# Performance work log

Hardware: AMD Instinct MI355X
Metric: run time of the kernel (lower is better)

Reference implementation:

```python
import jax, jax.numpy as jnp
import numpy as np

N, M, FEAT, GROUP, EMB = 512, 2048, 1024, 16, 64
DG = FEAT // GROUP  # 64 dims per head


def _make_boxes(k, n):
    k1, k2, k3, k4 = jax.random.split(k, 4)
    x = jax.random.uniform(k1, (n, 1)) * 800.0
    y = jax.random.uniform(k2, (n, 1)) * 800.0
    w = jax.random.uniform(k3, (n, 1)) * 120.0 + 16.0
    h = jax.random.uniform(k4, (n, 1)) * 120.0 + 16.0
    return jnp.concatenate([x, y, x + w, y + h], axis=1)


def setup_inputs() -> dict:
    key = jax.random.key(0)
    ks = jax.random.split(key, 10)
    std = 0.01
    fan = 1.0 / np.sqrt(FEAT).astype(np.float32)
    return {
        "bbox": _make_boxes(ks[0], N),
        "ref_bbox": _make_boxes(ks[1], M),
        "roi_feat": jax.random.normal(ks[2], (N, FEAT), dtype=jnp.float32),
        "ref_feat": jax.random.normal(ks[3], (M, FEAT), dtype=jnp.float32),
        "Wg_w": jax.random.normal(ks[4], (GROUP, EMB)) * std,
        "Wg_b": jnp.zeros((GROUP,), jnp.float32),
        "Wq_w": jax.random.normal(ks[5], (FEAT, FEAT)) * fan,
        "Wq_b": jnp.zeros((FEAT,), jnp.float32),
        "Wk_w": jax.random.normal(ks[6], (FEAT, FEAT)) * fan,
        "Wk_b": jnp.zeros((FEAT,), jnp.float32),
        "Wv_w": jax.random.normal(ks[7], (GROUP, DG, FEAT)) * std,
        "Wv_b": jnp.zeros((FEAT,), jnp.float32),
        "u": jax.random.normal(ks[8], (GROUP, 1, EMB)) * std,
    }


def _position_embedding(bbox, ref_bbox, feat_dim=64, wave_length=1000.0):
    # extract_position_matrix: geometry deltas between every (roi, ref) pair
    xr0, yr0, xr1, yr1 = jnp.split(ref_bbox, 4, axis=1)  # [M,1]
    wr = xr1 - xr0 + 1.0
    hr = yr1 - yr0 + 1.0
    cxr = 0.5 * (xr0 + xr1)
    cyr = 0.5 * (yr0 + yr1)
    x0, y0, x1, y1 = jnp.split(bbox, 4, axis=1)  # [N,1]
    w = x1 - x0 + 1.0
    h = y1 - y0 + 1.0
    cx = 0.5 * (x0 + x1)
    cy = 0.5 * (y0 + y1)
    dx = jnp.log(jnp.abs((cx - cxr.T) / w) + 1e-3)  # [N,M]
    dy = jnp.log(jnp.abs((cy - cyr.T) / h) + 1e-3)
    dw = jnp.log(w / wr.T)
    dh = jnp.log(h / hr.T)
    pos = jnp.stack([dx, dy, dw, dh], axis=2)  # [N,M,4]
    # extract_position_embedding: sinusoidal encoding, feat_dim/8 frequencies
    fr = jnp.arange(feat_dim // 8, dtype=pos.dtype)
    dim_mat = wave_length ** (8.0 / feat_dim * fr)  # [8]
    div = (pos[..., None] * 100.0) / dim_mat  # [N,M,4,8]
    emb = jnp.concatenate([jnp.sin(div), jnp.cos(div)], axis=3)  # [N,M,4,16]
    emb = emb.reshape(emb.shape[0], emb.shape[1], -1)  # [N,M,64]
    return jnp.transpose(emb, (2, 0, 1))  # [emb_dim, N, M]


def reference(bbox, ref_bbox, roi_feat, ref_feat, Wg_w, Wg_b, Wq_w, Wq_b,
              Wk_w, Wk_b, Wv_w, Wv_b, u):
    pe = _position_embedding(bbox, ref_bbox)  # [EMB, N, M]
    # Wg: 1x1 conv over embedding channels, relu -> attention prior weights
    pos_feat = jax.nn.relu(jnp.einsum('ge,enm->gnm', Wg_w, pe)
                           + Wg_b[:, None, None])  # [G,N,M]
    aff_weight = jnp.transpose(pos_feat, (1, 0, 2))  # [N,G,M]
    q = (roi_feat @ Wq_w.T + Wq_b).reshape(-1, GROUP, DG).transpose(1, 0, 2)  # [G,N,DG]
    k = (ref_feat @ Wk_w.T + Wk_b).reshape(-1, GROUP, DG).transpose(1, 0, 2)  # [G,M,DG]
    # content score + global content-bias (u) score, per head
    aff = jnp.einsum('gnd,gmd->gnm', q, k) + jnp.einsum('gld,gmd->glm', u, k)
    aff_scale = (aff / np.sqrt(float(DG))).transpose(1, 0, 2)  # [N,G,M]
    weighted_aff = jnp.log(aff_weight + 1e-6) + aff_scale
    attn = jax.nn.softmax(weighted_aff, axis=2)  # [N,G,M]
    out_t = jnp.einsum('ngm,mf->ngf', attn, ref_feat)  # [N,G,FEAT]
    # grouped 1x1 conv Wv: per-group weight [DG, FEAT]
    out = jnp.einsum('ngc,gdc->ngd', out_t, Wv_w).reshape(-1, FEAT) + Wv_b
    return out  # [N, FEAT]
```

## Files before the change

### kernel.cpp

```cpp
#include <hip/hip_runtime.h>
#include <stdint.h>

typedef float f32x4 __attribute__((ext_vector_type(4)));
typedef _Float16 f16x8 __attribute__((ext_vector_type(8)));
typedef _Float16 f16x4 __attribute__((ext_vector_type(4)));
typedef int int4v __attribute__((ext_vector_type(4)));

#define LOG2E 1.44269504088896340736f

__device__ __forceinline__ void gload_lds16(const void* g, void* l) {
    auto gp = reinterpret_cast<const uint32_t __attribute__((address_space(1)))*>(
        reinterpret_cast<uintptr_t>(g));
    auto lp = reinterpret_cast<uint32_t __attribute__((address_space(3)))*>(
        reinterpret_cast<uintptr_t>(l));
    __builtin_amdgcn_global_load_lds(gp, lp, 16, 0, 0);
}

__global__ __launch_bounds__(256) void mega_prep(
    const float* __restrict__ bbox, const float* __restrict__ ref_bbox,
    const float* __restrict__ roi_feat, const float* __restrict__ ref_feat,
    const float* __restrict__ Wg_w, const float* __restrict__ Wq_w,
    const float* __restrict__ Wk_w, const float* __restrict__ Wv_w,
    const float* __restrict__ Wq_b, const float* __restrict__ uvec,
    _Float16* __restrict__ roi_h, _Float16* __restrict__ ref_h,
    _Float16* __restrict__ wq_h, _Float16* __restrict__ wk_h,
    _Float16* __restrict__ wv_h, _Float16* __restrict__ wg_h,
    float* __restrict__ qbias, float* __restrict__ roig, float* __restrict__ refg)
{
    int idx = blockIdx.x * 256 + threadIdx.x;
    if (idx < 1442048) {
        const float* src; _Float16* dst; int off;
        if (idx < 131072)       { src = roi_feat; dst = roi_h; off = idx; }
        else if (idx < 655360)  { src = ref_feat; dst = ref_h; off = idx - 131072; }
        else if (idx < 917504)  { src = Wq_w;     dst = wq_h;  off = idx - 655360; }
        else if (idx < 1179648) { src = Wk_w;     dst = wk_h;  off = idx - 917504; }
        else if (idx < 1441792) { src = Wv_w;     dst = wv_h;  off = idx - 1179648; }
        else                    { src = Wg_w;     dst = wg_h;  off = idx - 1441792; }
        f32x4 v = *(const f32x4*)(src + (size_t)off * 4);
        f16x4 o;
        o[0] = (_Float16)v[0]; o[1] = (_Float16)v[1];
        o[2] = (_Float16)v[2]; o[3] = (_Float16)v[3];
        *(f16x4*)(dst + (size_t)off * 4) = o;
    } else if (idx < 1442304) {
        int off = idx - 1442048;
        f32x4 a = *(const f32x4*)(Wq_b + off * 4);
        f32x4 b = *(const f32x4*)(uvec + off * 4);
        f32x4 r = a + b;
        *(f32x4*)(qbias + off * 4) = r;
    } else if (idx < 1442816) {
        int n = idx - 1442304;
        f32x4 bb = *(const f32x4*)(bbox + n * 4);
        float w = bb[2] - bb[0] + 1.0f, h = bb[3] - bb[1] + 1.0f;
        f32x4 o1 = {0.5f*(bb[0]+bb[2]), 0.5f*(bb[1]+bb[3]), 1.0f/w, 1.0f/h};
        f32x4 o2 = {__logf(w), __logf(h), 0.f, 0.f};
        *(f32x4*)(roig + n*8) = o1;
        *(f32x4*)(roig + n*8 + 4) = o2;
    } else if (idx < 1444864) {
        int m = idx - 1442816;
        f32x4 bb = *(const f32x4*)(ref_bbox + m * 4);
        float w = bb[2] - bb[0] + 1.0f, h = bb[3] - bb[1] + 1.0f;
        f32x4 o = {0.5f*(bb[0]+bb[2]), 0.5f*(bb[1]+bb[3]), __logf(w), __logf(h)};
        *(f32x4*)(refg + m*4) = o;
    }
}

__global__ __launch_bounds__(256) void mega_gemm(
    const _Float16* __restrict__ roi_h, const _Float16* __restrict__ ref_h,
    const _Float16* __restrict__ wq_h, const _Float16* __restrict__ wk_h,
    const _Float16* __restrict__ wv_h, const float* __restrict__ qbias,
    const float* __restrict__ Wk_b,
    _Float16* __restrict__ Qg, _Float16* __restrict__ Kg, _Float16* __restrict__ Vth)
{
    __shared__ _Float16 As[64 * 32];
    __shared__ _Float16 Bs[128 * 32];

    int b = blockIdx.x;
    const _Float16 *A, *B;
    const float* bias;
    _Float16* out;
    int tm, tn, mode, MR; float scale;
    if (b < 64)       { A = roi_h; B = wq_h; bias = qbias; out = Qg;  tm = b >> 3;        tn = b & 7;       mode = 0; MR = 512;  scale = 0.125f * LOG2E; }
    else if (b < 320) { A = ref_h; B = wk_h; bias = Wk_b;  out = Kg;  tm = (b-64) >> 3;   tn = (b-64) & 7;  mode = 0; MR = 2048; scale = 1.f; }
    else              { A = ref_h; B = wv_h; bias = nullptr; out = Vth; tm = (b-320) >> 3; tn = (b-320) & 7; mode = 1; MR = 2048; scale = 1.f; }

    int tid = threadIdx.x;
    int w = tid >> 6, l = tid & 63, q = l >> 4, t = l & 15;
    int wm = w >> 1, wn = w & 1;
    int m0 = tm * 64, n0 = tn * 128;

    const _Float16* gA  = A + (size_t)(m0 + w*16 + (l >> 2)) * 1024 + (l & 3) * 8;
    const _Float16* gB  = B + (size_t)(n0 + w*16 + (l >> 2)) * 1024 + (l & 3) * 8;
    const _Float16* gB2 = gB + 64 * 1024;
    _Float16* lA  = &As[w * 512];
    _Float16* lB  = &Bs[w * 512];
    _Float16* lB2 = &Bs[2048 + w * 512];

    f32x4 acc[2][4];
    #pragma unroll
    for (int i = 0; i < 2; ++i)
        #pragma unroll
        for (int j = 0; j < 4; ++j)
            acc[i][j] = (f32x4){0.f, 0.f, 0.f, 0.f};

    for (int k0 = 0; k0 < 1024; k0 += 32) {
        gload_lds16(gA + k0, lA);
        gload_lds16(gB + k0, lB);
        gload_lds16(gB2 + k0, lB2);
        __syncthreads();
        f16x8 af[2], bfv[4];
        #pragma unroll
        for (int i = 0; i < 2; ++i)
            af[i]  = *(const f16x8*)&As[(wm*32 + i*16 + t) * 32 + q*8];
        #pragma unroll
        for (int j = 0; j < 4; ++j)
            bfv[j] = *(const f16x8*)&Bs[(wn*64 + j*16 + t) * 32 + q*8];
        #pragma unroll
        for (int mi = 0; mi < 2; ++mi)
            #pragma unroll
            for (int ni = 0; ni < 4; ++ni)
                acc[mi][ni] = __builtin_amdgcn_mfma_f32_16x16x32_f16(af[mi], bfv[ni], acc[mi][ni], 0, 0, 0);
        __syncthreads();
    }

    #pragma unroll
    for (int mi = 0; mi < 2; ++mi) {
        #pragma unroll
        for (int ni = 0; ni < 4; ++ni) {
            int col  = n0 + wn*64 + ni*16 + t;
            int row0 = m0 + wm*32 + mi*16 + q*4;
            f32x4 a = acc[mi][ni];
            if (mode == 0) {
                float bb = bias[col];
                _Float16* op = out + ((size_t)(col >> 6) * MR + row0) * 64 + (col & 63);
                #pragma unroll
                for (int r = 0; r < 4; ++r)
                    op[(size_t)r * 64] = (_Float16)((a[r] + bb) * scale);
            } else {
                f16x4 pk;
                pk[0] = (_Float16)a[0]; pk[1] = (_Float16)a[1];
                pk[2] = (_Float16)a[2]; pk[3] = (_Float16)a[3];
                *(f16x4*)(out + (size_t)col * 2048 + row0) = pk;
            }
        }
    }
}

__global__ __launch_bounds__(256) void mega_prior(
    const _Float16* __restrict__ wg_h, const float* __restrict__ Wg_b,
    const float* __restrict__ roig, const float* __restrict__ refg,
    _Float16* __restrict__ prior)
{
    int tid = threadIdx.x;
    int w = tid >> 6, l = tid & 63, q = l >> 4, p = l & 15;
    int n = blockIdx.x >> 1, half = blockIdx.x & 1;

    f16x8 wa0 = *(const f16x8*)(wg_h + p*64 + q*8);
    f16x8 wa1 = *(const f16x8*)(wg_h + p*64 + 32 + q*8);
    f32x4 wb = *(const f32x4*)(Wg_b + q*4);

    f32x4 rg1 = *(const f32x4*)(roig + n*8);
    f32x4 rg2 = *(const f32x4*)(roig + n*8 + 4);

    float cf[8];
    #pragma unroll
    for (int f = 0; f < 8; ++f)
        cf[f] = 15.9154943091895336f * __builtin_exp2f(-1.24572303558276059f * (float)f);

    float coff = (q & 1) ? 0.25f : 0.0f;
    bool isX = (q < 2);

    int mstart = half * 1024 + w * 256;
    for (int it = 0; it < 16; ++it) {
        int m = mstart + it * 16 + p;
        f32x4 rg = *(const f32x4*)(refg + m * 4);
        float posA = isX ? __logf(fabsf(rg1[0] - rg[0]) * rg1[2] + 1e-3f)
                         : __logf(fabsf(rg1[1] - rg[1]) * rg1[3] + 1e-3f);
        float posB = isX ? (rg2[0] - rg[2]) : (rg2[1] - rg[3]);
        f16x8 e0, e1;
        #pragma unroll
        for (int f = 0; f < 8; ++f) {
            float a0 = posA * cf[f] + coff; a0 -= floorf(a0);
            float a1 = posB * cf[f] + coff; a1 -= floorf(a1);
            e0[f] = (_Float16)__builtin_amdgcn_sinf(a0);
            e1[f] = (_Float16)__builtin_amdgcn_sinf(a1);
        }
        f32x4 acc = wb;
        acc = __builtin_amdgcn_mfma_f32_16x16x32_f16(wa0, e0, acc, 0, 0, 0);
        acc = __builtin_amdgcn_mfma_f32_16x16x32_f16(wa1, e1, acc, 0, 0, 0);
        _Float16* pp = prior + (size_t)n * 2048 + m;
        #pragma unroll
        for (int r = 0; r < 4; ++r)
            pp[(size_t)(q*4 + r) * 1048576] = (_Float16)fmaxf(acc[r], 0.f);
    }
}

#define SWZ(row, cb) ((cb) ^ (((row) & 7) << 4))

__device__ __forceinline__ f16x8 ld128s(const _Float16* base, int row, int cb) {
    return *(const f16x8*)((const char*)base + row * 128 + SWZ(row, cb));
}
__device__ __forceinline__ f16x4 ld64s(const _Float16* base, int row, int cb) {
    return *(const f16x4*)((const char*)base + row * 128 + SWZ(row, cb));
}

__global__ __launch_bounds__(256, 4) void mega_attn(
    const _Float16* __restrict__ Qg, const _Float16* __restrict__ Kg,
    const _Float16* __restrict__ Vth, const _Float16* __restrict__ prior,
    float* __restrict__ Opart, float* __restrict__ Mpart, float* __restrict__ Lpart)
{
    __shared__ __align__(16) _Float16 Kl[4096];
    __shared__ __align__(16) _Float16 Vl[4096];
    __shared__ __align__(16) _Float16 Pl[4096];

    int bid = blockIdx.x;
    int g = bid >> 6, nt4 = (bid >> 3) & 7, s = bid & 7;
    int tid = threadIdx.x;
    int w = tid >> 6, l = tid & 63, q = l >> 4, t = l & 15;
    int n0 = nt4 * 64, m0 = s * 256;

    int n = n0 + w * 16 + t;
    const _Float16* Qrow = Qg + ((size_t)g * 512 + n) * 64;
    f16x8 qf0 = *(const f16x8*)(Qrow + q * 8);
    f16x8 qf1 = *(const f16x8*)(Qrow + 32 + q * 8);

    int r_lo = tid >> 3, c8 = tid & 7;
    const char* gK = (const char*)(Kg + ((size_t)g * 2048 + m0) * 64);
    const char* gV = (const char*)(Vth + (size_t)g * 64 * 2048 + m0);
    const char* gP = (const char*)(prior + ((size_t)g * 512 + n0) * 2048 + m0);

    int4v kr0, kr1, vr0, vr1, pq0, pq1;
#define LOADC(c) { \
    kr0 = *(const int4v*)(gK + (c)*8192 + r_lo*128 + c8*16); \
    kr1 = *(const int4v*)(gK + (c)*8192 + (r_lo+32)*128 + c8*16); \
    vr0 = *(const int4v*)(gV + (c)*128 + (size_t)r_lo*4096 + c8*16); \
    vr1 = *(const int4v*)(gV + (c)*128 + (size_t)(r_lo+32)*4096 + c8*16); \
    pq0 = *(const int4v*)(gP + (c)*128 + (size_t)r_lo*4096 + c8*16); \
    pq1 = *(const int4v*)(gP + (c)*128 + (size_t)(r_lo+32)*4096 + c8*16); }
#define WRITEC() { \
    int cb = c8 * 16, sw = SWZ(r_lo, cb); \
    *(int4v*)((char*)Kl + r_lo*128 + sw) = kr0; \
    *(int4v*)((char*)Kl + (r_lo+32)*128 + sw) = kr1; \
    *(int4v*)((char*)Vl + r_lo*128 + sw) = vr0; \
    *(int4v*)((char*)Vl + (r_lo+32)*128 + sw) = vr1; \
    *(int4v*)((char*)Pl + r_lo*128 + sw) = pq0; \
    *(int4v*)((char*)Pl + (r_lo+32)*128 + sw) = pq1; }

    float mrow = -INFINITY, lsum = 0.f;
    f32x4 O0 = {0,0,0,0}, O1 = {0,0,0,0}, O2 = {0,0,0,0}, O3 = {0,0,0,0};

    LOADC(0);
    for (int c = 0; c < 4; ++c) {
        __syncthreads();
        WRITEC();
        __syncthreads();
        if (c < 3) LOADC(c + 1);

        f16x4 pr[4];
        #pragma unroll
        for (int mi = 0; mi < 4; ++mi)
            pr[mi] = ld64s(Pl, w * 16 + t, mi * 32 + q * 8);
        f32x4 sv[4];
        #pragma unroll
        for (int mi = 0; mi < 4; ++mi) {
            f16x8 k0 = ld128s(Kl, mi * 16 + t, q * 16);
            f16x8 k1 = ld128s(Kl, mi * 16 + t, 64 + q * 16);
            f32x4 z = {0, 0, 0, 0};
            z = __builtin_amdgcn_mfma_f32_16x16x32_f16(k0, qf0, z, 0, 0, 0);
            z = __builtin_amdgcn_mfma_f32_16x16x32_f16(k1, qf1, z, 0, 0, 0);
            sv[mi] = z;
        }
        #pragma unroll
        for (int mi = 0; mi < 4; ++mi)
            #pragma unroll
            for (int r = 0; r < 4; ++r)
                sv[mi][r] += __log2f((float)pr[mi][r] + 1e-6f);
        f16x4 vv[4][4];
        #pragma unroll
        for (int i = 0; i < 4; ++i)
            #pragma unroll
            for (int mi = 0; mi < 4; ++mi)
                vv[i][mi] = ld64s(Vl, i * 16 + t, mi * 32 + q * 8);
        float cmax = -INFINITY;
        #pragma unroll
        for (int mi = 0; mi < 4; ++mi)
            #pragma unroll
            for (int r = 0; r < 4; ++r)
                cmax = fmaxf(cmax, sv[mi][r]);
        cmax = fmaxf(cmax, __shfl_xor(cmax, 16));
        cmax = fmaxf(cmax, __shfl_xor(cmax, 32));
        float mnew = fmaxf(mrow, cmax);
        float corr = __builtin_exp2f(mrow - mnew);
        float psum = 0.f;
        f16x4 pf[4];
        #pragma unroll
        for (int mi = 0; mi < 4; ++mi) {
            #pragma unroll
            for (int r = 0; r < 4; ++r) {
                float pv = __builtin_exp2f(sv[mi][r] - mnew);
                psum += pv;
                pf[mi][r] = (_Float16)pv;
            }
        }
        psum += __shfl_xor(psum, 16);
        psum += __shfl_xor(psum, 32);
        lsum = lsum * corr + psum;
        mrow = mnew;
        O0 *= corr; O1 *= corr; O2 *= corr; O3 *= corr;
        #pragma unroll
        for (int mi = 0; mi < 4; ++mi) {
            O0 = __builtin_amdgcn_mfma_f32_16x16x16f16(vv[0][mi], pf[mi], O0, 0, 0, 0);
            O1 = __builtin_amdgcn_mfma_f32_16x16x16f16(vv[1][mi], pf[mi], O1, 0, 0, 0);
            O2 = __builtin_amdgcn_mfma_f32_16x16x16f16(vv[2][mi], pf[mi], O2, 0, 0, 0);
            O3 = __builtin_amdgcn_mfma_f32_16x16x16f16(vv[3][mi], pf[mi], O3, 0, 0, 0);
        }
    }
    int u = ((g * 32 + nt4 * 4 + w) << 3) + s;
    size_t ob = (size_t)(u * 16 + t) * 64;
    *(f32x4*)(Opart + ob + q*4)      = O0;
    *(f32x4*)(Opart + ob + 16 + q*4) = O1;
    *(f32x4*)(Opart + ob + 32 + q*4) = O2;
    *(f32x4*)(Opart + ob + 48 + q*4) = O3;
    if (q == 0) { Mpart[u*16 + t] = mrow; Lpart[u*16 + t] = lsum; }
#undef LOADC
#undef WRITEC
}

__global__ __launch_bounds__(256) void mega_combine(
    const float* __restrict__ Opart, const float* __restrict__ Mpart,
    const float* __restrict__ Lpart, const float* __restrict__ Wv_b,
    float* __restrict__ outp)
{
    int idx = blockIdx.x * 256 + threadIdx.x;
    int n = idx >> 10, col = idx & 1023;
    int g = col >> 6, d = col & 63;
    int nt = n >> 4, t = n & 15;
    int u0 = ((g * 32 + nt) << 3);
    float ms[8];
    #pragma unroll
    for (int s = 0; s < 8; ++s) ms[s] = Mpart[(u0 + s) * 16 + t];
    float M = ms[0];
    #pragma unroll
    for (int s = 1; s < 8; ++s) M = fmaxf(M, ms[s]);
    float accO = 0.f, accL = 0.f;
    #pragma unroll
    for (int s = 0; s < 8; ++s) {
        float wgt = __builtin_exp2f(ms[s] - M);
        accO += wgt * Opart[(size_t)((u0 + s) * 16 + t) * 64 + d];
        accL += wgt * Lpart[(u0 + s) * 16 + t];
    }
    outp[idx] = accO / accL + Wv_b[col];
}

extern "C" void kernel_launch(void* const* d_in, const int* in_sizes, int n_in,
                              void* d_out, int out_size, void* d_ws, size_t ws_size,
                              hipStream_t stream)
{
    const float* bbox     = (const float*)d_in[0];
    const float* ref_bbox = (const float*)d_in[1];
    const float* roi_feat = (const float*)d_in[2];
    const float* ref_feat = (const float*)d_in[3];
    const float* Wg_w = (const float*)d_in[4];
    const float* Wg_b = (const float*)d_in[5];
    const float* Wq_w = (const float*)d_in[6];
    const float* Wq_b = (const float*)d_in[7];
    const float* Wk_w = (const float*)d_in[8];
    const float* Wk_b = (const float*)d_in[9];
    const float* Wv_w = (const float*)d_in[10];
    const float* Wv_b = (const float*)d_in[11];
    const float* uvec = (const float*)d_in[12];
    float* outp = (float*)d_out;
    char* ws = (char*)d_ws;

    _Float16* prior = (_Float16*)ws;
    _Float16* roi_h = (_Float16*)(ws + 0);
    _Float16* ref_h = (_Float16*)(ws + (1ull<<20));
    _Float16* wq_h  = (_Float16*)(ws + (5ull<<20));
    _Float16* wk_h  = (_Float16*)(ws + (7ull<<20));
    _Float16* wv_h  = (_Float16*)(ws + (9ull<<20));
    size_t b2 = 32ull<<20;
    _Float16* wg_h  = (_Float16*)(ws + b2);
    float* qbias    = (float*)(ws + b2 + 4096);
    float* roig     = (float*)(ws + b2 + 8192);
    float* refg     = (float*)(ws + b2 + 24576);
    _Float16* Qh    = (_Float16*)(ws + b2 + 65536);
    _Float16* Kh    = (_Float16*)(ws + b2 + 65536 + (1ull<<20));
    _Float16* Vth   = (_Float16*)(ws + b2 + 65536 + (5ull<<20));
    float* Opart    = (float*)(ws + b2 + 65536 + (9ull<<20));
    float* Mpart    = (float*)(ws + b2 + 65536 + (25ull<<20));
    float* Lpart    = (float*)(ws + b2 + 65536 + (25ull<<20) + 262144);

    mega_prep<<<5644, 256, 0, stream>>>(bbox, ref_bbox, roi_feat, ref_feat,
        Wg_w, Wq_w, Wk_w, Wv_w, Wq_b, uvec,
        roi_h, ref_h, wq_h, wk_h, wv_h, wg_h, qbias, roig, refg);
    mega_gemm<<<576, 256, 0, stream>>>(roi_h, ref_h, wq_h, wk_h, wv_h,
        qbias, Wk_b, Qh, Kh, Vth);
    mega_prior<<<1024, 256, 0, stream>>>(wg_h, Wg_b, roig, refg, prior);
    mega_attn<<<1024, 256, 0, stream>>>(Qh, Kh, Vth, prior, Opart, Mpart, Lpart);
    mega_combine<<<2048, 256, 0, stream>>>(Opart, Mpart, Lpart, Wv_b, outp);
}
```

Baseline: 161.9 us.

## Double-buffer GEMM and attention LDS tiles, add setprio, store fp16 partials

The projection GEMM now uses a 64-wide K tile with two swizzled LDS buffers, prefetching the next tile through global_load_lds while the current one is consumed. This halves the number of barriers per K loop. The attention kernel double-buffers its K/V/prior tiles so one barrier per chunk replaces two. It also raises wave priority around its MFMA blocks and lowers occupancy to 3 blocks per CU to make room for the extra LDS. Attention partial outputs are stored as fp16 instead of fp32, halving combine traffic at some cost in precision.

```diff
diff --git a/kernel.cpp b/kernel.cpp
--- a/kernel.cpp
+++ b/kernel.cpp
@@ -71,8 +71,8 @@
     const float* __restrict__ Wk_b,
     _Float16* __restrict__ Qg, _Float16* __restrict__ Kg, _Float16* __restrict__ Vth)
 {
-    __shared__ _Float16 As[64 * 32];
-    __shared__ _Float16 Bs[128 * 32];
+    __shared__ __align__(16) _Float16 As[2][64 * 64];
+    __shared__ __align__(16) _Float16 Bs[2][128 * 64];
 
     int b = blockIdx.x;
     const _Float16 *A, *B;
@@ -88,12 +88,21 @@
     int wm = w >> 1, wn = w & 1;
     int m0 = tm * 64, n0 = tn * 128;
 
-    const _Float16* gA  = A + (size_t)(m0 + w*16 + (l >> 2)) * 1024 + (l & 3) * 8;
-    const _Float16* gB  = B + (size_t)(n0 + w*16 + (l >> 2)) * 1024 + (l & 3) * 8;
-    const _Float16* gB2 = gB + 64 * 1024;
-    _Float16* lA  = &As[w * 512];
-    _Float16* lB  = &Bs[w * 512];
-    _Float16* lB2 = &Bs[2048 + w * 512];
+    int r = tid >> 3, c8 = tid & 7;
+    int swz = (c8 * 16) ^ ((r & 7) << 4);
+    const char* gA = (const char*)A + (size_t)(m0 + r) * 2048 + swz;
+    const char* gB = (const char*)B + (size_t)(n0 + r) * 2048 + swz;
+    char* lA = (char*)&As[0][0] + (w * 8) * 128;
+    char* lB = (char*)&Bs[0][0] + (w * 8) * 128;
+
+#define GSTAGE(bufi, kt) { \
+    size_t ko = (size_t)(kt) * 128; \
+    gload_lds16(gA + ko,               lA + (bufi)*8192); \
+    gload_lds16(gA + ko + 32*2048,     lA + (bufi)*8192 + 32*128); \
+    gload_lds16(gB + ko,               lB + (bufi)*16384); \
+    gload_lds16(gB + ko + 32*2048,     lB + (bufi)*16384 + 32*128); \
+    gload_lds16(gB + ko + 64*2048,     lB + (bufi)*16384 + 64*128); \
+    gload_lds16(gB + ko + 96*2048,     lB + (bufi)*16384 + 96*128); }
 
     f32x4 acc[2][4];
     #pragma unroll
@@ -102,25 +111,42 @@
         for (int j = 0; j < 4; ++j)
             acc[i][j] = (f32x4){0.f, 0.f, 0.f, 0.f};
 
-    for (int k0 = 0; k0 < 1024; k0 += 32) {
-        gload_lds16(gA + k0, lA);
-        gload_lds16(gB + k0, lB);
-        gload_lds16(gB2 + k0, lB2);
+    GSTAGE(0, 0);
+    __syncthreads();
+
+    for (int kt = 0; kt < 16; ++kt) {
+        int cur = kt & 1;
+        if (kt < 15) GSTAGE(cur ^ 1, kt + 1);
+
+        const char* cA = (const char*)&As[0][0] + cur * 8192;
+        const char* cB = (const char*)&Bs[0][0] + cur * 16384;
+        f16x8 af[2][2], bf[2][4];
+        #pragma unroll
+        for (int mi = 0; mi < 2; ++mi) {
+            int row = wm * 32 + mi * 16 + t;
+            int sx = (row & 7) << 4;
+            #pragma unroll
+            for (int ks = 0; ks < 2; ++ks)
+                af[ks][mi] = *(const f16x8*)(cA + row * 128 + ((ks * 64 + q * 16) ^ sx));
+        }
+        #pragma unroll
+        for (int ni = 0; ni < 4; ++ni) {
+            int row = wn * 64 + ni * 16 + t;
+            int sx = (row & 7) << 4;
+            #pragma unroll
+            for (int ks = 0; ks < 2; ++ks)
+                bf[ks][ni] = *(const f16x8*)(cB + row * 128 + ((ks * 64 + q * 16) ^ sx));
+        }
+        #pragma unroll
+        for (int ks = 0; ks < 2; ++ks)
+            #pragma unroll
+            for (int mi = 0; mi < 2; ++mi)
+                #pragma unroll
+                for (int ni = 0; ni < 4; ++ni)
+                    acc[mi][ni] = __builtin_amdgcn_mfma_f32_16x16x32_f16(af[ks][mi], bf[ks][ni], acc[mi][ni], 0, 0, 0);
         __syncthreads();
-        f16x8 af[2], bfv[4];
-        #pragma unroll
-        for (int i = 0; i < 2; ++i)
-            af[i]  = *(const f16x8*)&As[(wm*32 + i*16 + t) * 32 + q*8];
-        #pragma unroll
-        for (int j = 0; j < 4; ++j)
-            bfv[j] = *(const f16x8*)&Bs[(wn*64 + j*16 + t) * 32 + q*8];
-        #pragma unroll
-        for (int mi = 0; mi < 2; ++mi)
-            #pragma unroll
-            for (int ni = 0; ni < 4; ++ni)
-                acc[mi][ni] = __builtin_amdgcn_mfma_f32_16x16x32_f16(af[mi], bfv[ni], acc[mi][ni], 0, 0, 0);
-        __syncthreads();
-    }
+    }
+#undef GSTAGE
 
     #pragma unroll
     for (int mi = 0; mi < 2; ++mi) {
@@ -133,8 +159,8 @@
                 float bb = bias[col];
                 _Float16* op = out + ((size_t)(col >> 6) * MR + row0) * 64 + (col & 63);
                 #pragma unroll
-                for (int r = 0; r < 4; ++r)
-                    op[(size_t)r * 64] = (_Float16)((a[r] + bb) * scale);
+                for (int rr = 0; rr < 4; ++rr)
+                    op[(size_t)rr * 64] = (_Float16)((a[rr] + bb) * scale);
             } else {
                 f16x4 pk;
                 pk[0] = (_Float16)a[0]; pk[1] = (_Float16)a[1];
@@ -203,14 +229,14 @@
     return *(const f16x4*)((const char*)base + row * 128 + SWZ(row, cb));
 }
 
-__global__ __launch_bounds__(256, 4) void mega_attn(
+__global__ __launch_bounds__(256, 3) void mega_attn(
     const _Float16* __restrict__ Qg, const _Float16* __restrict__ Kg,
     const _Float16* __restrict__ Vth, const _Float16* __restrict__ prior,
-    float* __restrict__ Opart, float* __restrict__ Mpart, float* __restrict__ Lpart)
-{
-    __shared__ __align__(16) _Float16 Kl[4096];
-    __shared__ __align__(16) _Float16 Vl[4096];
-    __shared__ __align__(16) _Float16 Pl[4096];
+    _Float16* __restrict__ Opart, float* __restrict__ Mpart, float* __restrict__ Lpart)
+{
+    __shared__ __align__(16) _Float16 Kl[2][4096];
+    __shared__ __align__(16) _Float16 Vl[2][4096];
+    __shared__ __align__(16) _Float16 Pl[2][4096];
 
     int bid = blockIdx.x;
     int g = bid >> 6, nt4 = (bid >> 3) & 7, s = bid & 7;
@@ -236,39 +262,46 @@
     vr1 = *(const int4v*)(gV + (c)*128 + (size_t)(r_lo+32)*4096 + c8*16); \
     pq0 = *(const int4v*)(gP + (c)*128 + (size_t)r_lo*4096 + c8*16); \
     pq1 = *(const int4v*)(gP + (c)*128 + (size_t)(r_lo+32)*4096 + c8*16); }
-#define WRITEC() { \
+#define WRITEC(bufi) { \
     int cb = c8 * 16, sw = SWZ(r_lo, cb); \
-    *(int4v*)((char*)Kl + r_lo*128 + sw) = kr0; \
-    *(int4v*)((char*)Kl + (r_lo+32)*128 + sw) = kr1; \
-    *(int4v*)((char*)Vl + r_lo*128 + sw) = vr0; \
-    *(int4v*)((char*)Vl + (r_lo+32)*128 + sw) = vr1; \
-    *(int4v*)((char*)Pl + r_lo*128 + sw) = pq0; \
-    *(int4v*)((char*)Pl + (r_lo+32)*128 + sw) = pq1; }
+    *(int4v*)((char*)&Kl[bufi][0] + r_lo*128 + sw) = kr0; \
+    *(int4v*)((char*)&Kl[bufi][0] + (r_lo+32)*128 + sw) = kr1; \
+    *(int4v*)((char*)&Vl[bufi][0] + r_lo*128 + sw) = vr0; \
+    *(int4v*)((char*)&Vl[bufi][0] + (r_lo+32)*128 + sw) = vr1; \
+    *(int4v*)((char*)&Pl[bufi][0] + r_lo*128 + sw) = pq0; \
+    *(int4v*)((char*)&Pl[bufi][0] + (r_lo+32)*128 + sw) = pq1; }
 
     float mrow = -INFINITY, lsum = 0.f;
     f32x4 O0 = {0,0,0,0}, O1 = {0,0,0,0}, O2 = {0,0,0,0}, O3 = {0,0,0,0};
 
     LOADC(0);
+    WRITEC(0);
+    __syncthreads();
+
     for (int c = 0; c < 4; ++c) {
-        __syncthreads();
-        WRITEC();
-        __syncthreads();
+        int cur = c & 1;
         if (c < 3) LOADC(c + 1);
 
+        const _Float16* Kb_l = &Kl[cur][0];
+        const _Float16* Vb_l = &Vl[cur][0];
+        const _Float16* Pb_l = &Pl[cur][0];
+
         f16x4 pr[4];
         #pragma unroll
         for (int mi = 0; mi < 4; ++mi)
-            pr[mi] = ld64s(Pl, w * 16 + t, mi * 32 + q * 8);
+            pr[mi] = ld64s(Pb_l, w * 16 + t, mi * 32 + q * 8);
         f32x4 sv[4];
+        __builtin_amdgcn_s_setprio(1);
         #pragma unroll
         for (int mi = 0; mi < 4; ++mi) {
-            f16x8 k0 = ld128s(Kl, mi * 16 + t, q * 16);
-            f16x8 k1 = ld128s(Kl, mi * 16 + t, 64 + q * 16);
+            f16x8 k0 = ld128s(Kb_l, mi * 16 + t, q * 16);
+            f16x8 k1 = ld128s(Kb_l, mi * 16 + t, 64 + q * 16);
             f32x4 z = {0, 0, 0, 0};
             z = __builtin_amdgcn_mfma_f32_16x16x32_f16(k0, qf0, z, 0, 0, 0);
             z = __builtin_amdgcn_mfma_f32_16x16x32_f16(k1, qf1, z, 0, 0, 0);
             sv[mi] = z;
         }
+        __builtin_amdgcn_s_setprio(0);
         #pragma unroll
         for (int mi = 0; mi < 4; ++mi)
             #pragma unroll
@@ -279,7 +312,7 @@
         for (int i = 0; i < 4; ++i)
             #pragma unroll
             for (int mi = 0; mi < 4; ++mi)
-                vv[i][mi] = ld64s(Vl, i * 16 + t, mi * 32 + q * 8);
+                vv[i][mi] = ld64s(Vb_l, i * 16 + t, mi * 32 + q * 8);
         float cmax = -INFINITY;
         #pragma unroll
         for (int mi = 0; mi < 4; ++mi)
@@ -306,6 +339,7 @@
         lsum = lsum * corr + psum;
         mrow = mnew;
         O0 *= corr; O1 *= corr; O2 *= corr; O3 *= corr;
+        __builtin_amdgcn_s_setprio(1);
         #pragma unroll
         for (int mi = 0; mi < 4; ++mi) {
             O0 = __builtin_amdgcn_mfma_f32_16x16x16f16(vv[0][mi], pf[mi], O0, 0, 0, 0);
@@ -313,20 +347,28 @@
             O2 = __builtin_amdgcn_mfma_f32_16x16x16f16(vv[2][mi], pf[mi], O2, 0, 0, 0);
             O3 = __builtin_amdgcn_mfma_f32_16x16x16f16(vv[3][mi], pf[mi], O3, 0, 0, 0);
         }
-    }
+        __builtin_amdgcn_s_setprio(0);
+
+        if (c < 3) WRITEC(cur ^ 1);
+        __syncthreads();
+    }
+
     int u = ((g * 32 + nt4 * 4 + w) << 3) + s;
     size_t ob = (size_t)(u * 16 + t) * 64;
-    *(f32x4*)(Opart + ob + q*4)      = O0;
-    *(f32x4*)(Opart + ob + 16 + q*4) = O1;
-    *(f32x4*)(Opart + ob + 32 + q*4) = O2;
-    *(f32x4*)(Opart + ob + 48 + q*4) = O3;
+    f16x4 ph;
+#define PK(O) { ph[0]=(_Float16)O[0]; ph[1]=(_Float16)O[1]; ph[2]=(_Float16)O[2]; ph[3]=(_Float16)O[3]; }
+    PK(O0) *(f16x4*)(Opart + ob + q*4)      = ph;
+    PK(O1) *(f16x4*)(Opart + ob + 16 + q*4) = ph;
+    PK(O2) *(f16x4*)(Opart + ob + 32 + q*4) = ph;
+    PK(O3) *(f16x4*)(Opart + ob + 48 + q*4) = ph;
+#undef PK
     if (q == 0) { Mpart[u*16 + t] = mrow; Lpart[u*16 + t] = lsum; }
 #undef LOADC
 #undef WRITEC
 }
 
 __global__ __launch_bounds__(256) void mega_combine(
-    const float* __restrict__ Opart, const float* __restrict__ Mpart,
+    const _Float16* __restrict__ Opart, const float* __restrict__ Mpart,
     const float* __restrict__ Lpart, const float* __restrict__ Wv_b,
     float* __restrict__ outp)
 {
@@ -345,7 +387,7 @@
     #pragma unroll
     for (int s = 0; s < 8; ++s) {
         float wgt = __builtin_exp2f(ms[s] - M);
-        accO += wgt * Opart[(size_t)((u0 + s) * 16 + t) * 64 + d];
+        accO += wgt * (float)Opart[(size_t)((u0 + s) * 16 + t) * 64 + d];
         accL += wgt * Lpart[(u0 + s) * 16 + t];
     }
     outp[idx] = accO / accL + Wv_b[col];
@@ -385,7 +427,7 @@
     _Float16* Qh    = (_Float16*)(ws + b2 + 65536);
     _Float16* Kh    = (_Float16*)(ws + b2 + 65536 + (1ull<<20));
     _Float16* Vth   = (_Float16*)(ws + b2 + 65536 + (5ull<<20));
-    float* Opart    = (float*)(ws + b2 + 65536 + (9ull<<20));
+    _Float16* Opart = (_Float16*)(ws + b2 + 65536 + (9ull<<20));
     float* Mpart    = (float*)(ws + b2 + 65536 + (25ull<<20));
     float* Lpart    = (float*)(ws + b2 + 65536 + (25ull<<20) + 262144);
 
```

Result: faster. 149.8 us (-7.5%).
